# Optimization experiments

Hardware: AMD Instinct MI355X
Metric: run time of the kernel (lower is better)

## Reference

```python
import jax, jax.numpy as jnp
import numpy as np

N_NODES = 32000
N_EDGES = 512000
F_IN = 128
HEADS = 4
CH = 64
NODES_PER_GRAPH = 500
BATCH = 64
HID = 512
ZDIM = 64


def _gat_layer(x, src, dst, W, att_src, att_dst, bias):
    # PyG GATConv, concat=True, negative_slope=0.2, self-loops already appended.
    N = x.shape[0]
    h = (x @ W).reshape(N, HEADS, CH)                 # [N,H,C]
    a_s = jnp.sum(h * att_src, axis=-1)               # [N,H]
    a_d = jnp.sum(h * att_dst, axis=-1)               # [N,H]
    e = jax.nn.leaky_relu(a_s[src] + a_d[dst], negative_slope=0.2)  # [E,H]
    m = jax.ops.segment_max(e, dst, num_segments=N)   # segment softmax over dst
    p = jnp.exp(e - m[dst])
    denom = jax.ops.segment_sum(p, dst, num_segments=N)
    alpha = p / denom[dst]                            # [E,H]
    out = jax.ops.segment_sum(h[src] * alpha[..., None], dst, num_segments=N)
    return out.reshape(N, HEADS * CH) + bias


def setup_inputs() -> dict:
    key = jax.random.key(0)
    ks = jax.random.split(key, 16)
    s = 0.02
    x = jax.random.normal(ks[0], (N_NODES, F_IN), jnp.float32)
    edge_index = jax.random.randint(ks[1], (2, N_EDGES), 0, N_NODES, jnp.int64)
    W1 = jax.random.normal(ks[2], (F_IN, HEADS * CH), jnp.float32) * s
    att_src1 = jax.random.normal(ks[3], (HEADS, CH), jnp.float32) * s
    att_dst1 = jax.random.normal(ks[4], (HEADS, CH), jnp.float32) * s
    b1 = jnp.zeros((HEADS * CH,), jnp.float32)
    W2 = jax.random.normal(ks[5], (HEADS * CH, HEADS * CH), jnp.float32) * s
    att_src2 = jax.random.normal(ks[6], (HEADS, CH), jnp.float32) * s
    att_dst2 = jax.random.normal(ks[7], (HEADS, CH), jnp.float32) * s
    b2 = jnp.zeros((HEADS * CH,), jnp.float32)
    We = jax.random.normal(ks[8], (NODES_PER_GRAPH * HEADS * CH, HID), jnp.float32) * 0.002
    be = jnp.zeros((HID,), jnp.float32)
    Wmu = jax.random.normal(ks[9], (HID, ZDIM), jnp.float32) * s
    bmu = jnp.zeros((ZDIM,), jnp.float32)
    Wvar = jax.random.normal(ks[10], (HID, ZDIM), jnp.float32) * s
    bvar = jnp.zeros((ZDIM,), jnp.float32)
    return {"x": x, "W1": W1, "att_src1": att_src1, "att_dst1": att_dst1, "b1": b1,
            "W2": W2, "att_src2": att_src2, "att_dst2": att_dst2, "b2": b2,
            "We": We, "be": be, "Wmu": Wmu, "bmu": bmu, "Wvar": Wvar, "bvar": bvar,
            "edge_index": edge_index, "batch": BATCH}


def reference(x, W1, att_src1, att_dst1, b1, W2, att_src2, att_dst2, b2,
              We, be, Wmu, bmu, Wvar, bvar, edge_index, batch):
    N = x.shape[0]
    loops = jnp.arange(N, dtype=edge_index.dtype)
    src = jnp.concatenate([edge_index[0], loops])
    dst = jnp.concatenate([edge_index[1], loops])
    h = jax.nn.relu(_gat_layer(x, src, dst, W1, att_src1, att_dst1, b1))
    h = jax.nn.relu(_gat_layer(h, src, dst, W2, att_src2, att_dst2, b2))
    xg = h.reshape(batch, -1)                         # [B, in_fea*H*C]
    y = xg @ We + be                                  # [B, HID]
    mu_b = jnp.mean(y, axis=0)                        # BatchNorm1d (training stats), eps=1e-3
    var_b = jnp.var(y, axis=0)
    y = (y - mu_b) / jnp.sqrt(var_b + 1e-3)
    mu_l = jnp.mean(y, axis=-1, keepdims=True)        # LayerNorm, no affine, eps=1e-5
    var_l = jnp.var(y, axis=-1, keepdims=True)
    y = (y - mu_l) / jnp.sqrt(var_l + 1e-5)
    y = jax.nn.relu(y)
    z_loc = y @ Wmu + bmu
    z_scale = jnp.exp(y @ Wvar + bvar) + 1e-4
    return (z_loc, z_scale)
```

## Files before the change

### kernel.cpp

```cpp
#include <hip/hip_runtime.h>
#include <math.h>

#define NN 32000
#define FIN 128
#define HC 256
#define NH 4
#define HIDD 512
#define BB 64
#define ZD 64
#define NSPLIT 250
#define KBCH 512
#define BNB 128

typedef __bf16 bf16x8 __attribute__((ext_vector_type(8)));
typedef float f32x4 __attribute__((ext_vector_type(4)));
typedef unsigned int uint;

__device__ inline float lrelu(float x){ return x > 0.f ? x : 0.2f*x; }
__device__ inline unsigned short f2b(float f){
  uint u = __float_as_uint(f);
  return (unsigned short)((u + 0x7FFFu + ((u >> 16) & 1u)) >> 16);
}
__device__ inline float b2f(unsigned short b){ return __uint_as_float(((uint)b) << 16); }
__device__ inline float blo(uint v){ return __uint_as_float(v << 16); }
__device__ inline float bhi(uint v){ return __uint_as_float(v & 0xffff0000u); }

__global__ void k_detect(const void* ei, int* flag){
  int t = threadIdx.x;
  int v = ((const int*)ei)[2*t + 1];
  unsigned long long b = __ballot(v == 0);
  if (t == 0) *flag = (b == ~0ULL) ? 1 : 0;
}

__global__ void k_cvt(const float* __restrict__ in, unsigned short* __restrict__ out, int n){
  int i = blockIdx.x*256 + threadIdx.x;
  if (i < n) out[i] = f2b(in[i]);
}

__global__ void k_cvtT2(const float* __restrict__ W1, unsigned short* __restrict__ Wt1,
                        const float* __restrict__ W2, unsigned short* __restrict__ Wt2){
  int n = blockIdx.x, k = threadIdx.x;
  if (blockIdx.y == 0){ if (k < FIN) Wt1[n*FIN + k] = f2b(W1[k*HC + n]); }
  else                 { Wt2[n*HC + k] = f2b(W2[k*HC + n]); }
}

__global__ void k_hist(const void* ei, const int* __restrict__ flag, int* counts, int E){
  int i = blockIdx.x*256 + threadIdx.x;
  if (i < E){
    int d = *flag ? (int)((const long long*)ei)[E + i] : ((const int*)ei)[E + i];
    atomicAdd(&counts[d], 1);
  }
}

__global__ __launch_bounds__(1024) void k_scan(const int* __restrict__ counts,
    int* __restrict__ offs, int* __restrict__ cursor, int n){
  __shared__ int sums[1024];
  int t = threadIdx.x;
  const int CHK = 32;
  int base = t * CHK;
  int s = 0;
  for (int i = 0; i < CHK; i++){ int idx = base + i; if (idx < n) s += counts[idx]; }
  sums[t] = s;
  __syncthreads();
  for (int off = 1; off < 1024; off <<= 1){
    int v = (t >= off) ? sums[t - off] : 0;
    __syncthreads();
    sums[t] += v;
    __syncthreads();
  }
  int run = (t == 0) ? 0 : sums[t-1];
  for (int i = 0; i < CHK; i++){
    int idx = base + i;
    if (idx < n){ offs[idx] = run; cursor[idx] = run; run += counts[idx]; }
  }
  if (t == 1023) offs[n] = sums[1023];
}

__global__ void k_fill(const void* ei, const int* __restrict__ flag,
                       int* __restrict__ cursor, int* __restrict__ col, int E){
  int i = blockIdx.x*256 + threadIdx.x;
  if (i < E){
    int s, d;
    if (*flag){ s = (int)((const long long*)ei)[i]; d = (int)((const long long*)ei)[E + i]; }
    else      { s = ((const int*)ei)[i];            d = ((const int*)ei)[E + i]; }
    int pos = atomicAdd(&cursor[d], 1);
    col[pos] = s;
  }
}

__global__ __launch_bounds__(256) void k_gemm_n(const unsigned short* __restrict__ A,
    const unsigned short* __restrict__ Wt, int K,
    const float* __restrict__ ws, const float* __restrict__ wd,
    unsigned short* __restrict__ out, float* __restrict__ a_s, float* __restrict__ a_d){
  __shared__ unsigned short As[64][40];
  __shared__ unsigned short Bs[256][40];
  int m0 = blockIdx.x * 64;
  int t = threadIdx.x;
  int w = t >> 6, lane = t & 63, l15 = lane & 15, l16 = lane >> 4;
  f32x4 acc[16];
  #pragma unroll
  for (int c = 0; c < 16; c++) acc[c] = (f32x4){0.f,0.f,0.f,0.f};

  for (int k0 = 0; k0 < K; k0 += 32){
    {
      int row = t >> 2, ko = (t & 3) * 8;
      *(uint4*)&As[row][ko] = *(const uint4*)&A[(size_t)(m0 + row)*K + k0 + ko];
    }
    {
      #pragma unroll
      for (int p = 0; p < 4; p++)
        *(uint4*)&Bs[t][p*8] = *(const uint4*)&Wt[(size_t)t*K + k0 + p*8];
    }
    __syncthreads();
    bf16x8 af = *(const bf16x8*)&As[w*16 + l15][l16*8];
    #pragma unroll
    for (int c = 0; c < 16; c++){
      bf16x8 bfr = *(const bf16x8*)&Bs[c*16 + l15][l16*8];
      acc[c] = __builtin_amdgcn_mfma_f32_16x16x32_bf16(af, bfr, acc[c], 0, 0, 0);
    }
    __syncthreads();
  }

  #pragma unroll
  for (int r = 0; r < 4; r++){
    int row = m0 + w*16 + l16*4 + r;
    float hs[NH] = {0,0,0,0}, hd[NH] = {0,0,0,0};
    #pragma unroll
    for (int c = 0; c < 16; c++){
      float v = acc[c][r];
      int colc = c*16 + l15;
      out[(size_t)row*HC + colc] = f2b(v);
      hs[c>>2] += v * ws[colc];
      hd[c>>2] += v * wd[colc];
    }
    #pragma unroll
    for (int h = 0; h < NH; h++){
      float s = hs[h], d = hd[h];
      #pragma unroll
      for (int o = 1; o < 16; o <<= 1){ s += __shfl_xor(s, o); d += __shfl_xor(d, o); }
      if (l15 == h){ a_s[row*NH + h] = s; a_d[row*NH + h] = d; }
    }
  }
}

__global__ __launch_bounds__(256) void k_agg(const unsigned short* __restrict__ hp,
    const int* __restrict__ col, const int* __restrict__ offs,
    const float* __restrict__ a_s, const float* __restrict__ a_d,
    const float* __restrict__ bias, unsigned short* __restrict__ outb){
  int n = blockIdx.x*4 + (threadIdx.x >> 6);
  int lane = threadIdx.x & 63;
  int g = lane >> 4, l16 = lane & 15;
  int h = l16 >> 2;
  int c0 = l16 * 16;
  int b0 = offs[n], b1 = offs[n+1];
  float adh = a_d[n*NH + h];
  float pself = expf(lrelu(a_s[n*NH + h] + adh));
  float den = 0.f;
  float ac[16];
  #pragma unroll
  for (int j = 0; j < 16; j++) ac[j] = 0.f;
  #pragma unroll 2
  for (int i = b0 + g; i < b1; i += 4){
    int s = col[i];
    float p = expf(lrelu(a_s[s*NH + h] + adh));
    den += p;
    uint4 v0 = *(const uint4*)&hp[(size_t)s*HC + c0];
    uint4 v1 = *(const uint4*)&hp[(size_t)s*HC + c0 + 8];
    ac[0] = fmaf(p, blo(v0.x), ac[0]);   ac[1] = fmaf(p, bhi(v0.x), ac[1]);
    ac[2] = fmaf(p, blo(v0.y), ac[2]);   ac[3] = fmaf(p, bhi(v0.y), ac[3]);
    ac[4] = fmaf(p, blo(v0.z), ac[4]);   ac[5] = fmaf(p, bhi(v0.z), ac[5]);
    ac[6] = fmaf(p, blo(v0.w), ac[6]);   ac[7] = fmaf(p, bhi(v0.w), ac[7]);
    ac[8] = fmaf(p, blo(v1.x), ac[8]);   ac[9] = fmaf(p, bhi(v1.x), ac[9]);
    ac[10]= fmaf(p, blo(v1.y), ac[10]);  ac[11]= fmaf(p, bhi(v1.y), ac[11]);
    ac[12]= fmaf(p, blo(v1.z), ac[12]);  ac[13]= fmaf(p, bhi(v1.z), ac[13]);
    ac[14]= fmaf(p, blo(v1.w), ac[14]);  ac[15]= fmaf(p, bhi(v1.w), ac[15]);
  }
  den += __shfl_xor(den, 16);  den += __shfl_xor(den, 32);
  #pragma unroll
  for (int j = 0; j < 16; j++){
    ac[j] += __shfl_xor(ac[j], 16);
    ac[j] += __shfl_xor(ac[j], 32);
  }
  den += pself;
  float r = 1.f / den;
  if (g == 0){
    uint4 hv0 = *(const uint4*)&hp[(size_t)n*HC + c0];
    uint4 hv1 = *(const uint4*)&hp[(size_t)n*HC + c0 + 8];
    float hvf[16] = {blo(hv0.x),bhi(hv0.x),blo(hv0.y),bhi(hv0.y),
                     blo(hv0.z),bhi(hv0.z),blo(hv0.w),bhi(hv0.w),
                     blo(hv1.x),bhi(hv1.x),blo(hv1.y),bhi(hv1.y),
                     blo(hv1.z),bhi(hv1.z),blo(hv1.w),bhi(hv1.w)};
    uint ov[8];
    #pragma unroll
    for (int j = 0; j < 8; j++){
      float e0 = fmaxf((pself*hvf[2*j]   + ac[2*j]  )*r + bias[c0+2*j],   0.f);
      float e1 = fmaxf((pself*hvf[2*j+1] + ac[2*j+1])*r + bias[c0+2*j+1], 0.f);
      ov[j] = ((uint)f2b(e1) << 16) | (uint)f2b(e0);
    }
    *(uint4*)&outb[(size_t)n*HC + c0]     = *(uint4*)&ov[0];
    *(uint4*)&outb[(size_t)n*HC + c0 + 8] = *(uint4*)&ov[4];
  }
}

__global__ __launch_bounds__(256) void k_gemm_big(const unsigned short* __restrict__ xg,
    const float* __restrict__ We, float* __restrict__ part){
  __shared__ unsigned short As[2][64][40];
  __shared__ unsigned short Bs[2][BNB][40];
  int n0 = blockIdx.x * BNB;
  int kc = blockIdx.y;
  int kbase = kc * KBCH;
  int t = threadIdx.x, w = t >> 6, lane = t & 63, l15 = lane & 15, l16 = lane >> 4;
  int cc = t & (BNB-1);
  int khalf = t >> 7;
  int arow = t >> 2, ako = (t & 3) * 8;
  const float* bptr = We + (size_t)(kbase + khalf*16)*HIDD + n0 + cc;
  const unsigned short* aptr = xg + (size_t)arow*128000 + kbase + ako;
  f32x4 acc[8];
  #pragma unroll
  for (int c = 0; c < 8; c++) acc[c] = (f32x4){0.f,0.f,0.f,0.f};

  float rv[16]; uint4 a4;
  #pragma unroll
  for (int mm = 0; mm < 16; mm++) rv[mm] = bptr[(size_t)mm*HIDD];
  a4 = *(const uint4*)aptr;

  int p = 0;
  for (int ks = 0; ks < KBCH; ks += 32){
    *(uint4*)&As[p][arow][ako] = a4;
    #pragma unroll
    for (int j = 0; j < 8; j++){
      uint pk = ((uint)f2b(rv[2*j+1]) << 16) | (uint)f2b(rv[2*j]);
      *(uint*)&Bs[p][cc][khalf*16 + 2*j] = pk;
    }
    __syncthreads();
    if (ks + 32 < KBCH){
      const float* bp2 = bptr + (size_t)(ks + 32)*HIDD;
      #pragma unroll
      for (int mm = 0; mm < 16; mm++) rv[mm] = bp2[(size_t)mm*HIDD];
      a4 = *(const uint4*)(aptr + ks + 32);
    }
    bf16x8 af = *(const bf16x8*)&As[p][w*16 + l15][l16*8];
    #pragma unroll
    for (int c = 0; c < 8; c++){
      bf16x8 bfr = *(const bf16x8*)&Bs[p][c*16 + l15][l16*8];
      acc[c] = __builtin_amdgcn_mfma_f32_16x16x32_bf16(af, bfr, acc[c], 0, 0, 0);
    }
    p ^= 1;
  }
  float* pbase = part + (size_t)kc*BB*HIDD;
  #pragma unroll
  for (int r = 0; r < 4; r++){
    int row = w*16 + l16*4 + r;
    #pragma unroll
    for (int c = 0; c < 8; c++)
      pbase[row*HIDD + n0 + c*16 + l15] = acc[c][r];
  }
}

__global__ void k_reduce(const float* __restrict__ part, const float* __restrict__ be,
                         float* __restrict__ y){
  int o = blockIdx.x*256 + threadIdx.x;
  float s = 0.f;
  #pragma unroll 5
  for (int k = 0; k < NSPLIT; k++) s += part[(size_t)k*BB*HIDD + o];
  y[o] = s + be[o & (HIDD-1)];
}

__global__ __launch_bounds__(64) void k_bn(const float* __restrict__ y,
    float* __restrict__ ybn){
  int colb = blockIdx.x, r = threadIdx.x;
  float v = y[(size_t)r*HIDD + colb];
  float s = v, s2 = v*v;
  #pragma unroll
  for (int o = 32; o; o >>= 1){ s += __shfl_down(s, o); s2 += __shfl_down(s2, o); }
  s = __shfl(s, 0); s2 = __shfl(s2, 0);
  float mean = s * (1.f/BB);
  float var = s2 * (1.f/BB) - mean*mean;
  ybn[(size_t)r*HIDD + colb] = (v - mean) * rsqrtf(var + 1e-3f);
}

__global__ __launch_bounds__(512) void k_lnheads(const float* __restrict__ ybn,
    const float* __restrict__ Wmu, const float* __restrict__ bmu,
    const float* __restrict__ Wvar, const float* __restrict__ bvar,
    float* __restrict__ out){
  __shared__ float ssum[8], ssq[8];
  __shared__ float yrow[HIDD];
  int row = blockIdx.x, t = threadIdx.x;
  float v = ybn[(size_t)row*HIDD + t];
  float s = v, s2 = v*v;
  #pragma unroll
  for (int o = 32; o; o >>= 1){ s += __shfl_down(s, o); s2 += __shfl_down(s2, o); }
  if ((t & 63) == 0){ ssum[t>>6] = s; ssq[t>>6] = s2; }
  __syncthreads();
  if (t == 0){
    float S = 0, S2 = 0;
    for (int i = 0; i < 8; i++){ S += ssum[i]; S2 += ssq[i]; }
    ssum[0] = S; ssq[0] = S2;
  }
  __syncthreads();
  float mean = ssum[0] * (1.f/HIDD);
  float var = ssq[0] * (1.f/HIDD) - mean*mean;
  yrow[t] = fmaxf((v - mean) * rsqrtf(var + 1e-5f), 0.f);
  __syncthreads();
  int o = t >> 2, kq = t & 3;
  const float* Wc = (o < ZD) ? Wmu : Wvar;
  int j = (o < ZD) ? o : o - ZD;
  float acc = 0.f;
  #pragma unroll 4
  for (int k = kq*128; k < kq*128 + 128; k++)
    acc = fmaf(yrow[k], Wc[(size_t)k*ZD + j], acc);
  acc += __shfl_down(acc, 1);
  acc += __shfl_down(acc, 2);
  if (kq == 0){
    if (o < ZD) out[row*ZD + o] = acc + bmu[o];
    else        out[BB*ZD + row*ZD + j] = expf(acc + bvar[j]) + 1e-4f;
  }
}

extern "C" void kernel_launch(void* const* d_in, const int* in_sizes, int n_in,
                              void* d_out, int out_size, void* d_ws, size_t ws_size,
                              hipStream_t stream){
  const float* x    = (const float*)d_in[0];
  const float* W1   = (const float*)d_in[1];
  const float* as1  = (const float*)d_in[2];
  const float* ad1  = (const float*)d_in[3];
  const float* b1   = (const float*)d_in[4];
  const float* W2   = (const float*)d_in[5];
  const float* as2  = (const float*)d_in[6];
  const float* ad2  = (const float*)d_in[7];
  const float* b2   = (const float*)d_in[8];
  const float* We   = (const float*)d_in[9];
  const float* be   = (const float*)d_in[10];
  const float* Wmu  = (const float*)d_in[11];
  const float* bmu  = (const float*)d_in[12];
  const float* Wvar = (const float*)d_in[13];
  const float* bvar = (const float*)d_in[14];
  const void*  ei   = d_in[15];
  int E = in_sizes[15] / 2;

  char* w = (char*)d_ws;
  auto alloc = [&](size_t bytes)->void*{
    void* p = (void*)w; w += (bytes + 255) & ~(size_t)255; return p;
  };
  unsigned short* gb   = (unsigned short*)alloc((size_t)NN*HC*2);
  unsigned short* ab   = (unsigned short*)alloc((size_t)NN*HC*2);
  unsigned short* xb   = (unsigned short*)alloc((size_t)NN*FIN*2);
  unsigned short* Wt1  = (unsigned short*)alloc((size_t)HC*FIN*2);
  unsigned short* Wt2  = (unsigned short*)alloc((size_t)HC*HC*2);
  float*    a_s    = (float*)alloc((size_t)NN*NH*4);
  float*    a_d    = (float*)alloc((size_t)NN*NH*4);
  int*      counts = (int*)alloc((size_t)NN*4);
  int*      offs   = (int*)alloc((size_t)(NN+1)*4);
  int*      cursor = (int*)alloc((size_t)NN*4);
  int*      col    = (int*)alloc((size_t)E*4);
  int*      flag   = (int*)alloc(256);
  float*    part   = (float*)alloc((size_t)NSPLIT*BB*HIDD*4);
  float*    y      = (float*)alloc((size_t)BB*HIDD*4);
  float*    ybn    = (float*)alloc((size_t)BB*HIDD*4);

  k_detect<<<1, 64, 0, stream>>>(ei, flag);

  hipMemsetAsync(counts, 0, (size_t)NN*4, stream);
  k_hist<<<(E + 255)/256, 256, 0, stream>>>(ei, flag, counts, E);
  k_scan<<<1, 1024, 0, stream>>>(counts, offs, cursor, NN);
  k_fill<<<(E + 255)/256, 256, 0, stream>>>(ei, flag, cursor, col, E);

  k_cvt<<<(NN*FIN + 255)/256, 256, 0, stream>>>(x, xb, NN*FIN);
  k_cvtT2<<<dim3(HC, 2), 256, 0, stream>>>(W1, Wt1, W2, Wt2);

  k_gemm_n<<<NN/64, 256, 0, stream>>>(xb, Wt1, FIN, as1, ad1, gb, a_s, a_d);
  k_agg<<<NN/4, 256, 0, stream>>>(gb, col, offs, a_s, a_d, b1, ab);

  k_gemm_n<<<NN/64, 256, 0, stream>>>(ab, Wt2, HC, as2, ad2, gb, a_s, a_d);
  k_agg<<<NN/4, 256, 0, stream>>>(gb, col, offs, a_s, a_d, b2, ab);

  k_gemm_big<<<dim3(HIDD/BNB, NSPLIT), 256, 0, stream>>>(ab, We, part);
  k_reduce<<<BB*HIDD/256, 256, 0, stream>>>(part, be, y);
  k_bn<<<HIDD, 64, 0, stream>>>(y, ybn);
  k_lnheads<<<BB, 512, 0, stream>>>(ybn, Wmu, bmu, Wvar, bvar, (float*)d_out);
}
```

Measured before the change: 360.3 us.

## Fuse prep kernels and split GAT aggregation across channel blocks

Merges the edge-format detection, count zeroing, x/W bf16 conversion and degree histogram into two launches, which cuts launch overhead and the memset. Separately, the aggregation kernel is split over a second grid dimension of 8 channel blocks, so each wavefront gathers 4 bytes per neighbor instead of 32 and holds 2 accumulators instead of 16. This gives much more parallelism and lower register pressure, but each block re-reads the CSR offsets, column indices and a_s values 8 times, and the gathers become narrower.

```diff
diff --git a/kernel.cpp b/kernel.cpp
--- a/kernel.cpp
+++ b/kernel.cpp
@@ -25,30 +25,36 @@
 __device__ inline float blo(uint v){ return __uint_as_float(v << 16); }
 __device__ inline float bhi(uint v){ return __uint_as_float(v & 0xffff0000u); }
 
-__global__ void k_detect(const void* ei, int* flag){
-  int t = threadIdx.x;
-  int v = ((const int*)ei)[2*t + 1];
-  unsigned long long b = __ballot(v == 0);
-  if (t == 0) *flag = (b == ~0ULL) ? 1 : 0;
-}
-
-__global__ void k_cvt(const float* __restrict__ in, unsigned short* __restrict__ out, int n){
-  int i = blockIdx.x*256 + threadIdx.x;
-  if (i < n) out[i] = f2b(in[i]);
-}
-
-__global__ void k_cvtT2(const float* __restrict__ W1, unsigned short* __restrict__ Wt1,
-                        const float* __restrict__ W2, unsigned short* __restrict__ Wt2){
-  int n = blockIdx.x, k = threadIdx.x;
-  if (blockIdx.y == 0){ if (k < FIN) Wt1[n*FIN + k] = f2b(W1[k*HC + n]); }
-  else                 { Wt2[n*HC + k] = f2b(W2[k*HC + n]); }
-}
-
-__global__ void k_hist(const void* ei, const int* __restrict__ flag, int* counts, int E){
-  int i = blockIdx.x*256 + threadIdx.x;
-  if (i < E){
-    int d = *flag ? (int)((const long long*)ei)[E + i] : ((const int*)ei)[E + i];
-    atomicAdd(&counts[d], 1);
+__global__ void k_prep0(const void* ei, int* flag, int* counts){
+  int b = blockIdx.x, t = threadIdx.x;
+  if (b == 0 && t < 64){
+    int v = ((const int*)ei)[2*t + 1];
+    unsigned long long bal = __ballot(v == 0);
+    if (t == 0) *flag = (bal == ~0ULL) ? 1 : 0;
+  }
+  for (int i = b*256 + t; i < NN; i += gridDim.x*256) counts[i] = 0;
+}
+
+__global__ void k_prep1(const float* __restrict__ x, unsigned short* __restrict__ xb,
+                        const float* __restrict__ W1, unsigned short* __restrict__ Wt1,
+                        const float* __restrict__ W2, unsigned short* __restrict__ Wt2,
+                        const void* ei, const int* __restrict__ flag,
+                        int* __restrict__ counts, int E){
+  int b = blockIdx.x, t = threadIdx.x;
+  if (b < 16000){
+    int i = b*256 + t;
+    xb[i] = f2b(x[i]);
+  } else if (b < 16512){
+    int bb = b - 16000;
+    int n = bb & 255, which = bb >> 8;
+    if (which == 0){ if (t < FIN) Wt1[n*FIN + t] = f2b(W1[t*HC + n]); }
+    else           { Wt2[n*HC + t] = f2b(W2[t*HC + n]); }
+  } else {
+    int i = (b - 16512)*256 + t;
+    if (i < E){
+      int d = *flag ? (int)((const long long*)ei)[E + i] : ((const int*)ei)[E + i];
+      atomicAdd(&counts[d], 1);
+    }
   }
 }
 
@@ -148,57 +154,34 @@
     const float* __restrict__ a_s, const float* __restrict__ a_d,
     const float* __restrict__ bias, unsigned short* __restrict__ outb){
   int n = blockIdx.x*4 + (threadIdx.x >> 6);
+  int cb = blockIdx.y;
+  int h = cb >> 1;
   int lane = threadIdx.x & 63;
   int g = lane >> 4, l16 = lane & 15;
-  int h = l16 >> 2;
-  int c0 = l16 * 16;
+  int c0 = cb*32 + l16*2;
   int b0 = offs[n], b1 = offs[n+1];
   float adh = a_d[n*NH + h];
   float pself = expf(lrelu(a_s[n*NH + h] + adh));
-  float den = 0.f;
-  float ac[16];
-  #pragma unroll
-  for (int j = 0; j < 16; j++) ac[j] = 0.f;
+  float den = 0.f, a0 = 0.f, a1 = 0.f;
   #pragma unroll 2
   for (int i = b0 + g; i < b1; i += 4){
     int s = col[i];
     float p = expf(lrelu(a_s[s*NH + h] + adh));
     den += p;
-    uint4 v0 = *(const uint4*)&hp[(size_t)s*HC + c0];
-    uint4 v1 = *(const uint4*)&hp[(size_t)s*HC + c0 + 8];
-    ac[0] = fmaf(p, blo(v0.x), ac[0]);   ac[1] = fmaf(p, bhi(v0.x), ac[1]);
-    ac[2] = fmaf(p, blo(v0.y), ac[2]);   ac[3] = fmaf(p, bhi(v0.y), ac[3]);
-    ac[4] = fmaf(p, blo(v0.z), ac[4]);   ac[5] = fmaf(p, bhi(v0.z), ac[5]);
-    ac[6] = fmaf(p, blo(v0.w), ac[6]);   ac[7] = fmaf(p, bhi(v0.w), ac[7]);
-    ac[8] = fmaf(p, blo(v1.x), ac[8]);   ac[9] = fmaf(p, bhi(v1.x), ac[9]);
-    ac[10]= fmaf(p, blo(v1.y), ac[10]);  ac[11]= fmaf(p, bhi(v1.y), ac[11]);
-    ac[12]= fmaf(p, blo(v1.z), ac[12]);  ac[13]= fmaf(p, bhi(v1.z), ac[13]);
-    ac[14]= fmaf(p, blo(v1.w), ac[14]);  ac[15]= fmaf(p, bhi(v1.w), ac[15]);
-  }
-  den += __shfl_xor(den, 16);  den += __shfl_xor(den, 32);
-  #pragma unroll
-  for (int j = 0; j < 16; j++){
-    ac[j] += __shfl_xor(ac[j], 16);
-    ac[j] += __shfl_xor(ac[j], 32);
-  }
+    uint v = *(const uint*)&hp[(size_t)s*HC + c0];
+    a0 = fmaf(p, blo(v), a0);
+    a1 = fmaf(p, bhi(v), a1);
+  }
+  den += __shfl_xor(den, 16); den += __shfl_xor(den, 32);
+  a0  += __shfl_xor(a0, 16);  a0  += __shfl_xor(a0, 32);
+  a1  += __shfl_xor(a1, 16);  a1  += __shfl_xor(a1, 32);
   den += pself;
   float r = 1.f / den;
   if (g == 0){
-    uint4 hv0 = *(const uint4*)&hp[(size_t)n*HC + c0];
-    uint4 hv1 = *(const uint4*)&hp[(size_t)n*HC + c0 + 8];
-    float hvf[16] = {blo(hv0.x),bhi(hv0.x),blo(hv0.y),bhi(hv0.y),
-                     blo(hv0.z),bhi(hv0.z),blo(hv0.w),bhi(hv0.w),
-                     blo(hv1.x),bhi(hv1.x),blo(hv1.y),bhi(hv1.y),
-                     blo(hv1.z),bhi(hv1.z),blo(hv1.w),bhi(hv1.w)};
-    uint ov[8];
-    #pragma unroll
-    for (int j = 0; j < 8; j++){
-      float e0 = fmaxf((pself*hvf[2*j]   + ac[2*j]  )*r + bias[c0+2*j],   0.f);
-      float e1 = fmaxf((pself*hvf[2*j+1] + ac[2*j+1])*r + bias[c0+2*j+1], 0.f);
-      ov[j] = ((uint)f2b(e1) << 16) | (uint)f2b(e0);
-    }
-    *(uint4*)&outb[(size_t)n*HC + c0]     = *(uint4*)&ov[0];
-    *(uint4*)&outb[(size_t)n*HC + c0 + 8] = *(uint4*)&ov[4];
+    uint hv = *(const uint*)&hp[(size_t)n*HC + c0];
+    float o0 = fmaxf((pself*blo(hv) + a0)*r + bias[c0],   0.f);
+    float o1 = fmaxf((pself*bhi(hv) + a1)*r + bias[c0+1], 0.f);
+    *(uint*)&outb[(size_t)n*HC + c0] = ((uint)f2b(o1) << 16) | (uint)f2b(o0);
   }
 }
 
@@ -358,21 +341,17 @@
   float*    y      = (float*)alloc((size_t)BB*HIDD*4);
   float*    ybn    = (float*)alloc((size_t)BB*HIDD*4);
 
-  k_detect<<<1, 64, 0, stream>>>(ei, flag);
-
-  hipMemsetAsync(counts, 0, (size_t)NN*4, stream);
-  k_hist<<<(E + 255)/256, 256, 0, stream>>>(ei, flag, counts, E);
+  k_prep0<<<125, 256, 0, stream>>>(ei, flag, counts);
+  k_prep1<<<16512 + (E + 255)/256, 256, 0, stream>>>(x, xb, W1, Wt1, W2, Wt2,
+                                                     ei, flag, counts, E);
   k_scan<<<1, 1024, 0, stream>>>(counts, offs, cursor, NN);
   k_fill<<<(E + 255)/256, 256, 0, stream>>>(ei, flag, cursor, col, E);
 
-  k_cvt<<<(NN*FIN + 255)/256, 256, 0, stream>>>(x, xb, NN*FIN);
-  k_cvtT2<<<dim3(HC, 2), 256, 0, stream>>>(W1, Wt1, W2, Wt2);
-
   k_gemm_n<<<NN/64, 256, 0, stream>>>(xb, Wt1, FIN, as1, ad1, gb, a_s, a_d);
-  k_agg<<<NN/4, 256, 0, stream>>>(gb, col, offs, a_s, a_d, b1, ab);
+  k_agg<<<dim3(NN/4, 8), 256, 0, stream>>>(gb, col, offs, a_s, a_d, b1, ab);
 
   k_gemm_n<<<NN/64, 256, 0, stream>>>(ab, Wt2, HC, as2, ad2, gb, a_s, a_d);
-  k_agg<<<NN/4, 256, 0, stream>>>(gb, col, offs, a_s, a_d, b2, ab);
+  k_agg<<<dim3(NN/4, 8), 256, 0, stream>>>(gb, col, offs, a_s, a_d, b2, ab);
 
   k_gemm_big<<<dim3(HIDD/BNB, NSPLIT), 256, 0, stream>>>(ab, We, part);
   k_reduce<<<BB*HIDD/256, 256, 0, stream>>>(part, be, y);
```

After: 494.2 us. +37.1%, slower.
